# Kernel tuning notes

Measured on AMD Instinct MI355X. Metric: run time of the kernel, lower is better.

## Reference

```python
import jax, jax.numpy as jnp
import numpy as np


def setup_inputs() -> dict:
    key = jax.random.key(0)
    k1, k2, k3 = jax.random.split(key, 3)
    x = jax.random.normal(k1, (8192, 4096), dtype=jnp.float32)
    # weight initialized in [0,1] per initialize_binary_range (trunc_normal a=0,b=1)
    weight = jax.random.uniform(k2, (4096, 4096), dtype=jnp.float32)
    bias = jax.random.normal(k3, (4096,), dtype=jnp.float32)
    return {"x": x, "weight": weight, "bias": bias}


def binarize_ste(w):
    # forward: clamp(round(w), 0, 1); backward: identity (straight-through)
    w_bin = jnp.clip(jnp.round(w), 0.0, 1.0)
    return w + jax.lax.stop_gradient(w_bin - w)


def reference(x, weight, bias):
    # F.linear(input, W, b) = x @ W.T + b, with binarized weight
    w_b = binarize_ste(weight)
    return jnp.einsum('ni,oi->no', x, w_b) + bias
```

## Files before the change

kernel.cpp:

```cpp
#include <hip/hip_runtime.h>
#include <stdint.h>

typedef __attribute__((ext_vector_type(4))) int int4v;


__device__ __forceinline__ int pack4_rn(float4 v, float s) {
    int a = __float2int_rn(v.x * s) & 0xff;
    int b = __float2int_rn(v.y * s) & 0xff;
    int c = __float2int_rn(v.z * s) & 0xff;
    int d = __float2int_rn(v.w * s) & 0xff;
    return a | (b << 8) | (c << 16) | (d << 24);
}

__device__ __forceinline__ int bin4(float4 v) {
    int a = (v.x > 0.5f) ? 1 : 0;
    int b = (v.y > 0.5f) ? 1 : 0;
    int c = (v.z > 0.5f) ? 1 : 0;
    int d = (v.w > 0.5f) ? 1 : 0;
    return a | (b << 8) | (c << 16) | (d << 24);
}


__global__ __launch_bounds__(256) void lb_quant_x(const float* __restrict__ x,
        signed char* __restrict__ xq, float* __restrict__ rscale, int K)
{
    const int row = blockIdx.x;
    const int tid = threadIdx.x;
    const float* xr = x + (size_t)row * K;

    float mx = 0.f;
    for (int i = tid * 4; i < K; i += 256 * 4) {
        float4 v = *(const float4*)(xr + i);
        mx = fmaxf(mx, fmaxf(fmaxf(fabsf(v.x), fabsf(v.y)),
                             fmaxf(fabsf(v.z), fabsf(v.w))));
    }
#pragma unroll
    for (int s = 32; s; s >>= 1) mx = fmaxf(mx, __shfl_xor(mx, s));
    __shared__ float wmax[4];
    if ((tid & 63) == 0) wmax[tid >> 6] = mx;
    __syncthreads();
    mx = fmaxf(fmaxf(wmax[0], wmax[1]), fmaxf(wmax[2], wmax[3]));

    const float s = (mx > 0.f) ? 127.f / mx : 0.f;
    if (tid == 0) rscale[row] = (mx > 0.f) ? mx * (1.f / 127.f) : 0.f;

    for (int i = tid * 16; i < K; i += 256 * 16) {
        float4 a = *(const float4*)(xr + i);
        float4 b = *(const float4*)(xr + i + 4);
        float4 c = *(const float4*)(xr + i + 8);
        float4 d = *(const float4*)(xr + i + 12);
        int4 o;
        o.x = pack4_rn(a, s); o.y = pack4_rn(b, s);
        o.z = pack4_rn(c, s); o.w = pack4_rn(d, s);
        *(int4*)(xq + (size_t)row * K + i) = o;
    }
}


__global__ void lb_bin_w8(const float* __restrict__ w, int4* __restrict__ wq, long n16) {
    long i = (long)blockIdx.x * blockDim.x + threadIdx.x;
    long stride = (long)gridDim.x * blockDim.x;
    for (; i < n16; i += stride) {
        const float4* p = (const float4*)w + i * 4;
        float4 v0 = p[0], v1 = p[1], v2 = p[2], v3 = p[3];
        int4 o;
        o.x = bin4(v0); o.y = bin4(v1); o.z = bin4(v2); o.w = bin4(v3);
        wq[i] = o;
    }
}


#define BM 256
#define BN 256
#define BK 64
#define TBYTES 16384

#define MFMA16H(MH) do { \
    __builtin_amdgcn_s_setprio(1); \
    _Pragma("unroll") \
    for (int m_ = 0; m_ < 4; ++m_) { \
      _Pragma("unroll") \
      for (int n_ = 0; n_ < 4; ++n_) { \
        acc[(MH)*4+m_][n_] = __builtin_amdgcn_mfma_i32_16x16x64_i8( \
            af[(MH)*4+m_], bf[n_], acc[(MH)*4+m_][n_], 0, 0, 0); \
      } \
    } \
    __builtin_amdgcn_s_setprio(0); \
} while (0)

#define PHASE_SYNC do { \
    __builtin_amdgcn_s_barrier(); \
    asm volatile("s_waitcnt lgkmcnt(0)" ::: "memory"); \
    __builtin_amdgcn_sched_barrier(0); \
} while (0)

__global__ __launch_bounds__(512, 2) void lb_gemm256_i8(
    const signed char* __restrict__ A,
    const signed char* __restrict__ B,
    const float* __restrict__ rscale,
    const float* __restrict__ bias,
    float* __restrict__ C,
    int M, int N, int K)
{
    __shared__ signed char ldsA[4 * TBYTES];
    __shared__ signed char ldsB[4 * TBYTES];

    const int tid  = threadIdx.x;
    const int lane = tid & 63;
    const int wave = tid >> 6;
    const int wr   = wave >> 2;
    const int wc   = wave & 3;

    int nwg = gridDim.x;
    int bid = blockIdx.x;
    bid = (bid & 7) * (nwg >> 3) + (bid >> 3);

    const int ntiles = N / BN;
    const int brow = (bid / ntiles) * BM;
    const int bcol = (bid % ntiles) * BN;

    const signed char* Abase = A + (size_t)brow * K;
    const signed char* Bbase = B + (size_t)bcol * K;

    const int srr = tid >> 2;
    const int sg  = tid & 3;
    auto stage = [&](const signed char* gbase, signed char* lbuf, int kt, int c) {
        int rr = c * 128 + srr;
        int gl = (sg - (rr >> 1)) & 3;
        const signed char* src = gbase + (size_t)rr * K + (size_t)kt * BK + gl * 16;
        signed char* dst = lbuf + c * 8192 + tid * 16;
        __builtin_amdgcn_global_load_lds(
            (const __attribute__((address_space(1))) void*)src,
            (__attribute__((address_space(3))) void*)dst, 16, 0, 0);
    };

    const int fr = lane & 15;
    const int fq = lane >> 4;
    const int sl = (fq + (fr >> 1)) & 3;

    int4v acc[8][4];
#pragma unroll
    for (int i = 0; i < 8; ++i)
#pragma unroll
        for (int j = 0; j < 4; ++j)
            acc[i][j] = (int4v){0, 0, 0, 0};

    const int nk = K / BK;

#pragma unroll
    for (int t = 0; t < 3; ++t) {
        stage(Bbase, &ldsB[t * TBYTES], t, 0); stage(Bbase, &ldsB[t * TBYTES], t, 1);
        stage(Abase, &ldsA[t * TBYTES], t, 0); stage(Abase, &ldsA[t * TBYTES], t, 1);
    }
    asm volatile("s_waitcnt vmcnt(8)" ::: "memory");
    __builtin_amdgcn_s_barrier();

    int4v af[8], bf[4];

    for (int t = 0; t < nk; ++t) {
        const int buf = t & 3;
        const signed char* ap = &ldsA[buf * TBYTES + (wr * 128 + fr) * 64];
        const signed char* bp = &ldsB[buf * TBYTES + (wc * 64 + fr) * 64];
        const bool pf = (t + 3 < nk);
        const int sb = (t + 3) & 3;

#pragma unroll
        for (int m = 0; m < 4; ++m) af[m] = *(const int4v*)(ap + m * 1024 + sl * 16);
#pragma unroll
        for (int n = 0; n < 4; ++n) bf[n] = *(const int4v*)(bp + n * 1024 + sl * 16);
        if (pf) { stage(Bbase, &ldsB[sb * TBYTES], t + 3, 0);
                  stage(Bbase, &ldsB[sb * TBYTES], t + 3, 1); }
        PHASE_SYNC;
        MFMA16H(0);

#pragma unroll
        for (int m = 4; m < 8; ++m) af[m] = *(const int4v*)(ap + m * 1024 + sl * 16);
        if (pf) { stage(Abase, &ldsA[sb * TBYTES], t + 3, 0);
                  stage(Abase, &ldsA[sb * TBYTES], t + 3, 1); }
        if (pf)               asm volatile("s_waitcnt vmcnt(8)" ::: "memory");
        else if (t == nk - 3) asm volatile("s_waitcnt vmcnt(4)" ::: "memory");
        else if (t == nk - 2) asm volatile("s_waitcnt vmcnt(0)" ::: "memory");
        PHASE_SYNC;
        MFMA16H(1);
    }

    float bn[4];
#pragma unroll
    for (int n = 0; n < 4; ++n)
        bn[n] = bias[bcol + wc * 64 + n * 16 + fr];

#pragma unroll
    for (int m = 0; m < 8; ++m) {
#pragma unroll
        for (int j = 0; j < 4; ++j) {
            int row = brow + wr * 128 + m * 16 + fq * 4 + j;
            float rs = rscale[row];
#pragma unroll
            for (int n = 0; n < 4; ++n) {
                int col = bcol + wc * 64 + n * 16 + fr;
                C[(size_t)row * N + col] = (float)acc[m][n][j] * rs + bn[n];
            }
        }
    }
}


__global__ __launch_bounds__(256) void lb_gemm_fb(
    const float* __restrict__ x, const float* __restrict__ w,
    const float* __restrict__ bias, float* __restrict__ C,
    int M, int N, int K)
{
    __shared__ float As[16][65];
    __shared__ float Bs[16][65];
    const int tid = threadIdx.x;
    const int tx = tid & 15, ty = tid >> 4;
    const int brow = blockIdx.y * 64, bcol = blockIdx.x * 64;

    float acc[4][4] = {};
    for (int kt = 0; kt < K; kt += 16) {
        for (int i = tid; i < 64 * 16; i += 256) {
            int r = i >> 4, k = i & 15;
            As[k][r] = x[(long)(brow + r) * K + kt + k];
        }
        for (int i = tid; i < 64 * 16; i += 256) {
            int n = i >> 4, k = i & 15;
            Bs[k][n] = (w[(long)(bcol + n) * K + kt + k] > 0.5f) ? 1.f : 0.f;
        }
        __syncthreads();
#pragma unroll
        for (int k = 0; k < 16; ++k) {
            float a[4], b[4];
#pragma unroll
            for (int i = 0; i < 4; ++i) a[i] = As[k][ty * 4 + i];
#pragma unroll
            for (int j = 0; j < 4; ++j) b[j] = Bs[k][tx * 4 + j];
#pragma unroll
            for (int i = 0; i < 4; ++i)
#pragma unroll
                for (int j = 0; j < 4; ++j)
                    acc[i][j] += a[i] * b[j];
        }
        __syncthreads();
    }
#pragma unroll
    for (int i = 0; i < 4; ++i)
#pragma unroll
        for (int j = 0; j < 4; ++j)
            C[(long)(brow + ty * 4 + i) * N + bcol + tx * 4 + j] = acc[i][j] + bias[bcol + tx * 4 + j];
}


extern "C" void kernel_launch(void* const* d_in, const int* in_sizes, int n_in,
                              void* d_out, int out_size, void* d_ws, size_t ws_size,
                              hipStream_t stream) {
    const float* x    = (const float*)d_in[0];
    const float* w    = (const float*)d_in[1];
    const float* bias = (const float*)d_in[2];
    float* out = (float*)d_out;

    const int N = in_sizes[2];
    const int K = in_sizes[1] / N;
    const int M = in_sizes[0] / K;

    const size_t need = (size_t)M * K + (size_t)N * K + (size_t)M * 4;
    const int ngrid = (M / BM) * (N / BN);
    const bool ok = (ws_size >= need) && (M % BM == 0) && (N % BN == 0)
                    && (K % BK == 0) && (K / BK >= 4) && (ngrid % 8 == 0);

    if (ok) {
        signed char* xq = (signed char*)d_ws;
        signed char* wq = xq + (size_t)M * K;
        float* rscale   = (float*)(wq + (size_t)N * K);

        lb_quant_x<<<M, 256, 0, stream>>>(x, xq, rscale, K);
        long nw16 = (long)N * K / 16;
        lb_bin_w8<<<2048, 256, 0, stream>>>(w, (int4*)wq, nw16);

        lb_gemm256_i8<<<dim3(ngrid), 512, 0, stream>>>(xq, wq, rscale, bias, out, M, N, K);
    } else {
        dim3 grid(N / 64, M / 64);
        lb_gemm_fb<<<grid, 256, 0, stream>>>(x, w, bias, out, M, N, K);
    }
}
```

Before: 188.5 us.

## Double-buffer MFMA fragments in registers and unroll the K loop by two

Restructures the int8 GEMM main loop so each tile's LDS fragments for the next K step are loaded into a second register set while the current step's 32 MFMAs run. The previous two-phase-per-tile schedule with two barriers is replaced by one barrier per tile, and the vmcnt waits are adjusted to match. This aims to hide LDS read latency behind MFMA work and cut synchronisation. In exchange it doubles fragment register usage, which risks spills or lower occupancy under the 512x2 launch bounds, and it now requires K to be a multiple of 128.

```diff
diff --git a/kernel.cpp b/kernel.cpp
--- a/kernel.cpp
+++ b/kernel.cpp
@@ -75,23 +75,42 @@
 #define BK 64
 #define TBYTES 16384
 
-#define MFMA16H(MH) do { \
+#define PHASE_END(T) do { \
+    asm volatile("s_waitcnt lgkmcnt(0)" ::: "memory"); \
+    __builtin_amdgcn_sched_barrier(0); \
+    if ((T) + 3 < nk)           asm volatile("s_waitcnt vmcnt(4)" ::: "memory"); \
+    else if ((T) == nk - 3)     asm volatile("s_waitcnt vmcnt(0)" ::: "memory"); \
+    __builtin_amdgcn_s_barrier(); \
+} while (0)
+
+#define TILE_BODY(CUR, NXT, T) do { \
+    if ((T) + 3 < nk) { \
+        const int sb_ = ((T) + 3) & 3; \
+        stage(Bbase, &ldsB[sb_ * TBYTES], (T) + 3, 0); \
+        stage(Bbase, &ldsB[sb_ * TBYTES], (T) + 3, 1); \
+        stage(Abase, &ldsA[sb_ * TBYTES], (T) + 3, 0); \
+        stage(Abase, &ldsA[sb_ * TBYTES], (T) + 3, 1); \
+    } \
+    if ((T) + 1 < nk) { \
+        const int rb_ = ((T) + 1) & 3; \
+        const signed char* ap_ = &ldsA[rb_ * TBYTES + (wr * 128 + fr) * 64]; \
+        const signed char* bp_ = &ldsB[rb_ * TBYTES + (wc * 64 + fr) * 64]; \
+        _Pragma("unroll") \
+        for (int m_ = 0; m_ < 8; ++m_) fA[NXT][m_] = *(const int4v*)(ap_ + m_ * 1024 + sl * 16); \
+        _Pragma("unroll") \
+        for (int n_ = 0; n_ < 4; ++n_) fB[NXT][n_] = *(const int4v*)(bp_ + n_ * 1024 + sl * 16); \
+    } \
     __builtin_amdgcn_s_setprio(1); \
     _Pragma("unroll") \
-    for (int m_ = 0; m_ < 4; ++m_) { \
+    for (int m_ = 0; m_ < 8; ++m_) { \
       _Pragma("unroll") \
       for (int n_ = 0; n_ < 4; ++n_) { \
-        acc[(MH)*4+m_][n_] = __builtin_amdgcn_mfma_i32_16x16x64_i8( \
-            af[(MH)*4+m_], bf[n_], acc[(MH)*4+m_][n_], 0, 0, 0); \
+        acc[m_][n_] = __builtin_amdgcn_mfma_i32_16x16x64_i8( \
+            fA[CUR][m_], fB[CUR][n_], acc[m_][n_], 0, 0, 0); \
       } \
     } \
     __builtin_amdgcn_s_setprio(0); \
-} while (0)
-
-#define PHASE_SYNC do { \
-    __builtin_amdgcn_s_barrier(); \
-    asm volatile("s_waitcnt lgkmcnt(0)" ::: "memory"); \
-    __builtin_amdgcn_sched_barrier(0); \
+    if ((T) + 1 < nk) PHASE_END(T); \
 } while (0)
 
 __global__ __launch_bounds__(512, 2) void lb_gemm256_i8(
@@ -152,36 +171,22 @@
         stage(Bbase, &ldsB[t * TBYTES], t, 0); stage(Bbase, &ldsB[t * TBYTES], t, 1);
         stage(Abase, &ldsA[t * TBYTES], t, 0); stage(Abase, &ldsA[t * TBYTES], t, 1);
     }
-    asm volatile("s_waitcnt vmcnt(8)" ::: "memory");
+    asm volatile("s_waitcnt vmcnt(4)" ::: "memory");
     __builtin_amdgcn_s_barrier();
 
-    int4v af[8], bf[4];
-
-    for (int t = 0; t < nk; ++t) {
-        const int buf = t & 3;
-        const signed char* ap = &ldsA[buf * TBYTES + (wr * 128 + fr) * 64];
-        const signed char* bp = &ldsB[buf * TBYTES + (wc * 64 + fr) * 64];
-        const bool pf = (t + 3 < nk);
-        const int sb = (t + 3) & 3;
-
-#pragma unroll
-        for (int m = 0; m < 4; ++m) af[m] = *(const int4v*)(ap + m * 1024 + sl * 16);
-#pragma unroll
-        for (int n = 0; n < 4; ++n) bf[n] = *(const int4v*)(bp + n * 1024 + sl * 16);
-        if (pf) { stage(Bbase, &ldsB[sb * TBYTES], t + 3, 0);
-                  stage(Bbase, &ldsB[sb * TBYTES], t + 3, 1); }
-        PHASE_SYNC;
-        MFMA16H(0);
-
-#pragma unroll
-        for (int m = 4; m < 8; ++m) af[m] = *(const int4v*)(ap + m * 1024 + sl * 16);
-        if (pf) { stage(Abase, &ldsA[sb * TBYTES], t + 3, 0);
-                  stage(Abase, &ldsA[sb * TBYTES], t + 3, 1); }
-        if (pf)               asm volatile("s_waitcnt vmcnt(8)" ::: "memory");
-        else if (t == nk - 3) asm volatile("s_waitcnt vmcnt(4)" ::: "memory");
-        else if (t == nk - 2) asm volatile("s_waitcnt vmcnt(0)" ::: "memory");
-        PHASE_SYNC;
-        MFMA16H(1);
+    int4v fA[2][8], fB[2][4];
+    {
+        const signed char* ap_ = &ldsA[(wr * 128 + fr) * 64];
+        const signed char* bp_ = &ldsB[(wc * 64 + fr) * 64];
+#pragma unroll
+        for (int m_ = 0; m_ < 8; ++m_) fA[0][m_] = *(const int4v*)(ap_ + m_ * 1024 + sl * 16);
+#pragma unroll
+        for (int n_ = 0; n_ < 4; ++n_) fB[0][n_] = *(const int4v*)(bp_ + n_ * 1024 + sl * 16);
+    }
+
+    for (int t = 0; t < nk; t += 2) {
+        TILE_BODY(0, 1, t);
+        TILE_BODY(1, 0, t + 1);
     }
 
     float bn[4];
@@ -265,7 +270,7 @@
     const size_t need = (size_t)M * K + (size_t)N * K + (size_t)M * 4;
     const int ngrid = (M / BM) * (N / BN);
     const bool ok = (ws_size >= need) && (M % BM == 0) && (N % BN == 0)
-                    && (K % BK == 0) && (K / BK >= 4) && (ngrid % 8 == 0);
+                    && (K % (2 * BK) == 0) && (K / BK >= 4) && (ngrid % 8 == 0);
 
     if (ok) {
         signed char* xq = (signed char*)d_ws;
```

New measurement: 227.0 us. 20.5% more time.

## Shrink int8 GEMM tile to 256x128 with double buffering for more occupancy

Applied to the files above, without the earlier changes.

Replaces the 256x256 block tile and 4-stage LDS pipeline with a 256x128 tile, a 2-stage double-buffered pipeline and a single barrier-synchronised MFMA phase per k-step. Waves are rearranged 4x2, each still computing a 64x64 sub-tile. Launch bounds now request 4 blocks per CU. The aim is lower LDS and register use per block so more blocks can overlap latency. The cost is less data reuse per loaded tile, more global traffic, and a shallower prefetch depth.

```diff
diff --git a/kernel.cpp b/kernel.cpp
--- a/kernel.cpp
+++ b/kernel.cpp
@@ -71,30 +71,12 @@
 
 
 #define BM 256
-#define BN 256
+#define BN 128
 #define BK 64
-#define TBYTES 16384
-
-#define MFMA16H(MH) do { \
-    __builtin_amdgcn_s_setprio(1); \
-    _Pragma("unroll") \
-    for (int m_ = 0; m_ < 4; ++m_) { \
-      _Pragma("unroll") \
-      for (int n_ = 0; n_ < 4; ++n_) { \
-        acc[(MH)*4+m_][n_] = __builtin_amdgcn_mfma_i32_16x16x64_i8( \
-            af[(MH)*4+m_], bf[n_], acc[(MH)*4+m_][n_], 0, 0, 0); \
-      } \
-    } \
-    __builtin_amdgcn_s_setprio(0); \
-} while (0)
-
-#define PHASE_SYNC do { \
-    __builtin_amdgcn_s_barrier(); \
-    asm volatile("s_waitcnt lgkmcnt(0)" ::: "memory"); \
-    __builtin_amdgcn_sched_barrier(0); \
-} while (0)
-
-__global__ __launch_bounds__(512, 2) void lb_gemm256_i8(
+#define ATB 16384
+#define BTB 8192
+
+__global__ __launch_bounds__(512, 4) void lb_gemm_i8(
     const signed char* __restrict__ A,
     const signed char* __restrict__ B,
     const float* __restrict__ rscale,
@@ -102,14 +84,14 @@
     float* __restrict__ C,
     int M, int N, int K)
 {
-    __shared__ signed char ldsA[4 * TBYTES];
-    __shared__ signed char ldsB[4 * TBYTES];
+    __shared__ signed char ldsA[2 * ATB];
+    __shared__ signed char ldsB[2 * BTB];
 
     const int tid  = threadIdx.x;
     const int lane = tid & 63;
     const int wave = tid >> 6;
-    const int wr   = wave >> 2;
-    const int wc   = wave & 3;
+    const int wr   = wave >> 1;
+    const int wc   = wave & 1;
 
     int nwg = gridDim.x;
     int bid = blockIdx.x;
@@ -138,9 +120,9 @@
     const int fq = lane >> 4;
     const int sl = (fq + (fr >> 1)) & 3;
 
-    int4v acc[8][4];
-#pragma unroll
-    for (int i = 0; i < 8; ++i)
+    int4v acc[4][4];
+#pragma unroll
+    for (int i = 0; i < 4; ++i)
 #pragma unroll
         for (int j = 0; j < 4; ++j)
             acc[i][j] = (int4v){0, 0, 0, 0};
@@ -148,40 +130,49 @@
     const int nk = K / BK;
 
 #pragma unroll
-    for (int t = 0; t < 3; ++t) {
-        stage(Bbase, &ldsB[t * TBYTES], t, 0); stage(Bbase, &ldsB[t * TBYTES], t, 1);
-        stage(Abase, &ldsA[t * TBYTES], t, 0); stage(Abase, &ldsA[t * TBYTES], t, 1);
-    }
-    asm volatile("s_waitcnt vmcnt(8)" ::: "memory");
+    for (int t = 0; t < 2; ++t) {
+        stage(Abase, &ldsA[t * ATB], t, 0);
+        stage(Abase, &ldsA[t * ATB], t, 1);
+        stage(Bbase, &ldsB[t * BTB], t, 0);
+    }
+    asm volatile("s_waitcnt vmcnt(3)" ::: "memory");
     __builtin_amdgcn_s_barrier();
 
-    int4v af[8], bf[4];
+    int4v af[4], bf[4];
 
     for (int t = 0; t < nk; ++t) {
-        const int buf = t & 3;
-        const signed char* ap = &ldsA[buf * TBYTES + (wr * 128 + fr) * 64];
-        const signed char* bp = &ldsB[buf * TBYTES + (wc * 64 + fr) * 64];
-        const bool pf = (t + 3 < nk);
-        const int sb = (t + 3) & 3;
+        const int p = t & 1;
+        const signed char* ap = &ldsA[p * ATB + (wr * 64 + fr) * 64];
+        const signed char* bp = &ldsB[p * BTB + (wc * 64 + fr) * 64];
 
 #pragma unroll
         for (int m = 0; m < 4; ++m) af[m] = *(const int4v*)(ap + m * 1024 + sl * 16);
 #pragma unroll
         for (int n = 0; n < 4; ++n) bf[n] = *(const int4v*)(bp + n * 1024 + sl * 16);
-        if (pf) { stage(Bbase, &ldsB[sb * TBYTES], t + 3, 0);
-                  stage(Bbase, &ldsB[sb * TBYTES], t + 3, 1); }
-        PHASE_SYNC;
-        MFMA16H(0);
-
-#pragma unroll
-        for (int m = 4; m < 8; ++m) af[m] = *(const int4v*)(ap + m * 1024 + sl * 16);
-        if (pf) { stage(Abase, &ldsA[sb * TBYTES], t + 3, 0);
-                  stage(Abase, &ldsA[sb * TBYTES], t + 3, 1); }
-        if (pf)               asm volatile("s_waitcnt vmcnt(8)" ::: "memory");
-        else if (t == nk - 3) asm volatile("s_waitcnt vmcnt(4)" ::: "memory");
-        else if (t == nk - 2) asm volatile("s_waitcnt vmcnt(0)" ::: "memory");
-        PHASE_SYNC;
-        MFMA16H(1);
+        asm volatile("s_waitcnt lgkmcnt(0)" ::: "memory");
+        __builtin_amdgcn_sched_barrier(0);
+        __builtin_amdgcn_s_barrier();
+
+        if (t + 2 < nk) {
+            stage(Abase, &ldsA[p * ATB], t + 2, 0);
+            stage(Abase, &ldsA[p * ATB], t + 2, 1);
+            stage(Bbase, &ldsB[p * BTB], t + 2, 0);
+        }
+
+        __builtin_amdgcn_s_setprio(1);
+#pragma unroll
+        for (int m = 0; m < 4; ++m)
+#pragma unroll
+            for (int n = 0; n < 4; ++n)
+                acc[m][n] = __builtin_amdgcn_mfma_i32_16x16x64_i8(
+                    af[m], bf[n], acc[m][n], 0, 0, 0);
+        __builtin_amdgcn_s_setprio(0);
+
+        if (t < nk - 1) {
+            if (t + 2 < nk) asm volatile("s_waitcnt vmcnt(3)" ::: "memory");
+            else            asm volatile("s_waitcnt vmcnt(0)" ::: "memory");
+            __builtin_amdgcn_s_barrier();
+        }
     }
 
     float bn[4];
@@ -190,10 +181,10 @@
         bn[n] = bias[bcol + wc * 64 + n * 16 + fr];
 
 #pragma unroll
-    for (int m = 0; m < 8; ++m) {
+    for (int m = 0; m < 4; ++m) {
 #pragma unroll
         for (int j = 0; j < 4; ++j) {
-            int row = brow + wr * 128 + m * 16 + fq * 4 + j;
+            int row = brow + wr * 64 + m * 16 + fq * 4 + j;
             float rs = rscale[row];
 #pragma unroll
             for (int n = 0; n < 4; ++n) {
@@ -276,7 +267,7 @@
         long nw16 = (long)N * K / 16;
         lb_bin_w8<<<2048, 256, 0, stream>>>(w, (int4*)wq, nw16);
 
-        lb_gemm256_i8<<<dim3(ngrid), 512, 0, stream>>>(xq, wq, rscale, bias, out, M, N, K);
+        lb_gemm_i8<<<dim3(ngrid), 512, 0, stream>>>(xq, wq, rscale, bias, out, M, N, K);
     } else {
         dim3 grid(N / 64, M / 64);
         lb_gemm_fb<<<grid, 256, 0, stream>>>(x, w, bias, out, M, N, K);
```

New measurement: 191.2 us. Within noise of the previous version (+1.4%).
